# Kernel optimization log

Hardware: AMD Instinct MI355X
Metric: run time of the kernel (lower is better)

Reference implementation:

```python
import jax, jax.numpy as jnp
import numpy as np

DEPTH, DIM, HEADS, MLP, P, G, NCLS = 12, 768, 12, 3072, 16, 14, 1000
N = G * G + 1  # 197 tokens (cls + patches)
HD = DIM // HEADS
EPS = 1e-6


def _ln(x, g, b):
    m = jnp.mean(x, axis=-1, keepdims=True)
    v = jnp.var(x, axis=-1, keepdims=True)
    return (x - m) * jax.lax.rsqrt(v + EPS) * g + b


def setup_inputs() -> dict:
    key = jax.random.key(0)
    ks = jax.random.split(key, 16)
    d = {}
    d["x"] = jax.random.normal(ks[0], (32, 3, 224, 224), jnp.float32)
    d["cp_mask"] = jax.random.uniform(ks[1], (1, 1, N, N), jnp.float32)
    # patch embed conv (kernel [DIM, 3, P, P]) flattened to a matmul over (c, kh, kw)
    d["patch_w"] = jax.random.normal(ks[2], (3 * P * P, DIM), jnp.float32) * 0.02
    d["patch_b"] = jnp.zeros((DIM,), jnp.float32)
    d["cls_token"] = jax.random.normal(ks[3], (1, 1, DIM), jnp.float32) * 1e-6
    d["pos_embed"] = jax.random.normal(ks[4], (1, N, DIM), jnp.float32) * 0.02
    d["ln1_g"] = jnp.ones((DEPTH, DIM), jnp.float32)
    d["ln1_b"] = jnp.zeros((DEPTH, DIM), jnp.float32)
    d["qkv_w"] = jax.random.normal(ks[5], (DEPTH, DIM, 3 * DIM), jnp.float32) * 0.02
    d["qkv_b"] = jnp.zeros((DEPTH, 3 * DIM), jnp.float32)
    d["proj_w"] = jax.random.normal(ks[6], (DEPTH, DIM, DIM), jnp.float32) * 0.02
    d["proj_b"] = jnp.zeros((DEPTH, DIM), jnp.float32)
    d["ln2_g"] = jnp.ones((DEPTH, DIM), jnp.float32)
    d["ln2_b"] = jnp.zeros((DEPTH, DIM), jnp.float32)
    d["fc1_w"] = jax.random.normal(ks[7], (DEPTH, DIM, MLP), jnp.float32) * 0.02
    d["fc1_b"] = jnp.zeros((DEPTH, MLP), jnp.float32)
    d["fc2_w"] = jax.random.normal(ks[8], (DEPTH, MLP, DIM), jnp.float32) * 0.02
    d["fc2_b"] = jnp.zeros((DEPTH, DIM), jnp.float32)
    d["normf_g"] = jnp.ones((DIM,), jnp.float32)
    d["normf_b"] = jnp.zeros((DIM,), jnp.float32)
    d["head_w"] = jax.random.normal(ks[9], (DIM, NCLS), jnp.float32) * 0.02
    d["head_b"] = jnp.zeros((NCLS,), jnp.float32)
    return d


def vit_forward(x, cp_mask, patch_w, patch_b, cls_token, pos_embed,
                ln1_g, ln1_b, qkv_w, qkv_b, proj_w, proj_b,
                ln2_g, ln2_b, fc1_w, fc1_b, fc2_w, fc2_b,
                normf_g, normf_b, head_w, head_b):
    B = x.shape[0]
    scale = HD ** (-0.5)
    # PatchEmbed: stride-P conv == extract non-overlapping patches then matmul
    # [B,3,224,224] -> [B,3,G,P,G,P] -> [B,G,G,3,P,P] -> [B,196,3*P*P]
    patches = x.reshape(B, 3, G, P, G, P).transpose(0, 2, 4, 1, 3, 5).reshape(B, G * G, 3 * P * P)
    t = patches @ patch_w + patch_b  # [B,196,DIM]
    t = jnp.concatenate([jnp.broadcast_to(cls_token, (B, 1, DIM)), t], axis=1)
    t = t + pos_embed  # [B,197,DIM]

    for i in range(DEPTH):
        h = _ln(t, ln1_g[i], ln1_b[i])
        qkv = (h @ qkv_w[i] + qkv_b[i]).reshape(B, N, 3, HEADS, HD)
        q = qkv[:, :, 0].transpose(0, 2, 1, 3)  # [B,H,N,hd]
        k = qkv[:, :, 1].transpose(0, 2, 1, 3)
        v = qkv[:, :, 2].transpose(0, 2, 1, 3)
        attn = jnp.einsum('bhqd,bhkd->bhqk', q, k) * scale * cp_mask
        attn = jax.nn.softmax(attn, axis=-1)
        o = jnp.einsum('bhqk,bhkd->bhqd', attn, v).transpose(0, 2, 1, 3).reshape(B, N, DIM)
        t = t + (o @ proj_w[i] + proj_b[i])
        h = _ln(t, ln2_g[i], ln2_b[i])
        h = jax.nn.gelu(h @ fc1_w[i] + fc1_b[i], approximate=False)
        t = t + (h @ fc2_w[i] + fc2_b[i])

    t = _ln(t, normf_g, normf_b)
    pooled = t[:, 0]  # global_pool == 'token'
    return pooled @ head_w + head_b  # [B, NCLS]


def reference(x, cp_mask, patch_w, patch_b, cls_token, pos_embed,
              ln1_g, ln1_b, qkv_w, qkv_b, proj_w, proj_b,
              ln2_g, ln2_b, fc1_w, fc1_b, fc2_w, fc2_b,
              normf_g, normf_b, head_w, head_b):
    return vit_forward(x, cp_mask, patch_w, patch_b, cls_token, pos_embed,
                       ln1_g, ln1_b, qkv_w, qkv_b, proj_w, proj_b,
                       ln2_g, ln2_b, fc1_w, fc1_b, fc2_w, fc2_b,
                       normf_g, normf_b, head_w, head_b)
```

## Files before the change

kernel.cpp:

```cpp
#include <hip/hip_runtime.h>
#include <math.h>

#define BATCH 32
#define DEPTH 12
#define DIM 768
#define HEADS 12
#define MLP_DIM 3072
#define PATCH 16
#define GRIDSZ 14
#define NCLS 1000
#define N_TOK 197
#define HD 64
#define NPATCH 196

typedef __attribute__((ext_vector_type(8))) short short8;
typedef __attribute__((ext_vector_type(4))) float floatx4;
typedef unsigned short ushort;

__device__ inline float us2f(ushort u) {
    union { unsigned int i; float f; } c; c.i = ((unsigned int)u) << 16; return c.f;
}
__device__ inline ushort f2bf(float f) {
    unsigned int x = __float_as_uint(f);
    unsigned int r = (x + 0x7fffu + ((x >> 16) & 1u)) >> 16;
    return (ushort)r;
}

#define GAS __attribute__((address_space(1)))
#define LAS __attribute__((address_space(3)))
__device__ inline void async_copy16(const void* g, void* l) {
    __builtin_amdgcn_global_load_lds((const GAS void*)g, (LAS void*)l, 16, 0, 0);
}

__global__ __launch_bounds__(256) void im2col_kernel(const float* __restrict__ x,
                                                     ushort* __restrict__ patches) {
    int idx = blockIdx.x * 256 + threadIdx.x;
    const int total = BATCH * NPATCH * DIM;
    if (idx >= total) return;
    int e = idx % DIM;
    int n = (idx / DIM) % NPATCH;
    int b = idx / (DIM * NPATCH);
    int c = e / (PATCH * PATCH);
    int r = e % (PATCH * PATCH);
    int py = r / PATCH, px = r % PATCH;
    int gy = n / GRIDSZ, gx = n % GRIDSZ;
    size_t xi = (((size_t)(b * 3 + c) * 224 + gy * PATCH + py)) * 224 + gx * PATCH + px;
    patches[idx] = f2bf(x[xi]);
}

__global__ __launch_bounds__(256) void assemble_kernel(const float* __restrict__ patchout,
                                                       const float* __restrict__ cls,
                                                       const float* __restrict__ pos,
                                                       float* __restrict__ t) {
    int idx = blockIdx.x * 256 + threadIdx.x;
    const int total = BATCH * N_TOK * DIM;
    if (idx >= total) return;
    int d = idx % DIM;
    int n = (idx / DIM) % N_TOK;
    int b = idx / (DIM * N_TOK);
    float v = (n == 0) ? cls[d] : patchout[((size_t)b * NPATCH + (n - 1)) * DIM + d];
    t[idx] = v + pos[n * DIM + d];
}

__global__ __launch_bounds__(256) void lnw_kernel(const float* __restrict__ x,
                                                  const float* __restrict__ g,
                                                  const float* __restrict__ bta,
                                                  ushort* __restrict__ out,
                                                  int rows, int in_stride, int out_stride) {
    int w = threadIdx.x >> 6, l = threadIdx.x & 63;
    int row = blockIdx.x * 4 + w;
    if (row >= rows) return;
    const float* xr = x + (size_t)row * in_stride;
    float4 v[3];
    float s = 0.0f, s2 = 0.0f;
#pragma unroll
    for (int c = 0; c < 3; c++) {
        v[c] = *(const float4*)(xr + c * 256 + l * 4);
        s  += v[c].x + v[c].y + v[c].z + v[c].w;
        s2 += v[c].x * v[c].x + v[c].y * v[c].y + v[c].z * v[c].z + v[c].w * v[c].w;
    }
#pragma unroll
    for (int off = 32; off; off >>= 1) { s += __shfl_xor(s, off); s2 += __shfl_xor(s2, off); }
    float mean = s * (1.0f / DIM);
    float inv = rsqrtf(s2 * (1.0f / DIM) - mean * mean + 1e-6f);
    ushort* orow = out + (size_t)row * out_stride;
#pragma unroll
    for (int c = 0; c < 3; c++) {
        float4 gg = *(const float4*)(g + c * 256 + l * 4);
        float4 bb = *(const float4*)(bta + c * 256 + l * 4);
        ushort4 o4;
        o4.x = f2bf((v[c].x - mean) * inv * gg.x + bb.x);
        o4.y = f2bf((v[c].y - mean) * inv * gg.y + bb.y);
        o4.z = f2bf((v[c].z - mean) * inv * gg.z + bb.z);
        o4.w = f2bf((v[c].w - mean) * inv * gg.w + bb.w);
        *(ushort4*)(orow + c * 256 + l * 4) = o4;
    }
}

__global__ __launch_bounds__(256) void transpose_bf16_kernel(const float* __restrict__ in,
                                                             ushort* __restrict__ out,
                                                             int K, int N) {
    __shared__ float tile[32][33];
    int n0 = blockIdx.x * 32, k0 = blockIdx.y * 32;
    int tx = threadIdx.x;
    int ty = threadIdx.y;
    for (int r = ty; r < 32; r += 8) {
        int k = k0 + r, n = n0 + tx;
        tile[r][tx] = (k < K && n < N) ? in[(size_t)k * N + n] : 0.0f;
    }
    __syncthreads();
    for (int r = ty; r < 32; r += 8) {
        int n = n0 + r, k = k0 + tx;
        if (n < N && k < K) out[(size_t)n * K + k] = f2bf(tile[tx][r]);
    }
}

__global__ __launch_bounds__(256) void transpose4_kernel(
    const float* __restrict__ w0, const float* __restrict__ w1,
    const float* __restrict__ w2, const float* __restrict__ w3,
    ushort* __restrict__ o0, ushort* __restrict__ o1,
    ushort* __restrict__ o2, ushort* __restrict__ o3) {
    __shared__ float tile[32][33];
    int bid = blockIdx.x;
    const float* in; ushort* out; int K, N, nx, tl;
    if (bid < 1728)      { in = w0; out = o0; K = 768;  N = 2304; nx = 72; tl = bid; }
    else if (bid < 2304) { in = w1; out = o1; K = 768;  N = 768;  nx = 24; tl = bid - 1728; }
    else if (bid < 4608) { in = w2; out = o2; K = 768;  N = 3072; nx = 96; tl = bid - 2304; }
    else                 { in = w3; out = o3; K = 3072; N = 768;  nx = 24; tl = bid - 4608; }
    int n0 = (tl % nx) * 32, k0 = (tl / nx) * 32;
    int tx = threadIdx.x, ty = threadIdx.y;
    for (int r = ty; r < 32; r += 8)
        tile[r][tx] = in[(size_t)(k0 + r) * N + n0 + tx];
    __syncthreads();
    for (int r = ty; r < 32; r += 8)
        out[(size_t)(n0 + r) * K + k0 + tx] = f2bf(tile[tx][r]);
}

template <int BM, int GELU, int RES, int WF32, int WBF16>
__global__ __launch_bounds__(256) void gemm_bf16_mfma(
    const ushort* __restrict__ A, const ushort* __restrict__ Wt,
    const float* __restrict__ bias, const float* __restrict__ res,
    float* __restrict__ Cf, ushort* __restrict__ Cb,
    int M, int N, int K) {
    constexpr int WN = (BM == 128) ? 2 : 4;
    constexpr int FN = (BM == 128) ? 4 : 2;
    constexpr int AROWS = BM / 4;
    __shared__ short Asm[BM * 64];
    __shared__ short Bsm[128 * 64];
    const int tid = threadIdx.x;
    const int w = tid >> 6, lane = tid & 63;
    const int wm = w / WN, wn = w % WN;

    int gX = gridDim.x, gY = gridDim.y;
    int pid = blockIdx.y * gX + blockIdx.x;
    int width = 8 * gX;
    int group = pid / width;
    int first = group * 8;
    int gsz = min(gY - first, 8);
    int by = first + (pid % gsz);
    int bx = (pid % width) / gsz;
    const int m0 = by * BM, n0 = bx * 128;

    floatx4 acc[4][FN] = {};

    const int ro = lane >> 3;
    const int sl = lane & 7;
    const int gch = sl ^ ro;
    const ushort* aptr[BM / 32];
    short* alds[BM / 32];
#pragma unroll
    for (int i = 0; i < BM / 32; i++) {
        int r = w * AROWS + i * 8 + ro;
        int gr = min(m0 + r, M - 1);
        aptr[i] = A + (size_t)gr * K + gch * 8;
        alds[i] = Asm + (w * AROWS + i * 8) * 64;
    }
    const ushort* bptr[4];
    short* blds[4];
#pragma unroll
    for (int i = 0; i < 4; i++) {
        int r = w * 32 + i * 8 + ro;
        int gr = min(n0 + r, N - 1);
        bptr[i] = Wt + (size_t)gr * K + gch * 8;
        blds[i] = Bsm + (w * 32 + i * 8) * 64;
    }

    const int fr = lane & 15, quad = lane >> 4;

    for (int k0 = 0; k0 < K; k0 += 64) {
#pragma unroll
        for (int i = 0; i < BM / 32; i++) async_copy16(aptr[i] + k0, alds[i]);
#pragma unroll
        for (int i = 0; i < 4; i++) async_copy16(bptr[i] + k0, blds[i]);
        __syncthreads();
#pragma unroll
        for (int ks = 0; ks < 2; ks++) {
            int soff = (((ks * 4 + quad) ^ (fr & 7)) * 8);
            short8 af[4], bf[FN];
#pragma unroll
            for (int mt = 0; mt < 4; mt++)
                af[mt] = *(const short8*)&Asm[(wm * 64 + mt * 16 + fr) * 64 + soff];
#pragma unroll
            for (int nt = 0; nt < FN; nt++)
                bf[nt] = *(const short8*)&Bsm[(wn * (16 * FN) + nt * 16 + fr) * 64 + soff];
#pragma unroll
            for (int mt = 0; mt < 4; mt++)
#pragma unroll
                for (int nt = 0; nt < FN; nt++)
                    acc[mt][nt] = __builtin_amdgcn_mfma_f32_16x16x32_bf16(af[mt], bf[nt], acc[mt][nt], 0, 0, 0);
        }
        __syncthreads();
    }

#pragma unroll
    for (int nt = 0; nt < FN; nt++) {
        int col = n0 + wn * (16 * FN) + nt * 16 + fr;
        if (col >= N) continue;
        float bv = bias[col];
#pragma unroll
        for (int mt = 0; mt < 4; mt++) {
            int rbase = m0 + wm * 64 + mt * 16 + quad * 4;
#pragma unroll
            for (int r = 0; r < 4; r++) {
                int row = rbase + r;
                if (row >= M) continue;
                float v = acc[mt][nt][r] + bv;
                if (GELU) v = 0.5f * v * (1.0f + erff(v * 0.70710678118654752f));
                if (RES) v += res[(size_t)row * N + col];
                if (WF32) Cf[(size_t)row * N + col] = v;
                if (WBF16) Cb[(size_t)row * N + col] = f2bf(v);
            }
        }
    }
}

__global__ __launch_bounds__(256, 2) void attn_kernel(const ushort* __restrict__ qkvb,
                                                      const float* __restrict__ mask,
                                                      ushort* __restrict__ o) {
    const int h = blockIdx.x, b = blockIdx.y;
    const int tid = threadIdx.x;
    __shared__ ushort Vfrag[7 * 4 * 64 * 8];
    __shared__ ushort Pfrag[4 * 7 * 64 * 8];

    {
        uint4 z = {0, 0, 0, 0};
        uint4* v4 = (uint4*)Vfrag;
        uint4* p4 = (uint4*)Pfrag;
        for (int i = tid; i < 1792; i += 256) { v4[i] = z; p4[i] = z; }
    }
    __syncthreads();

    for (int pass = 0; pass < 25; pass++) {
        int j = pass * 8 + (tid >> 5);
        if (j <= 196) {
            int d0 = (tid & 31) * 2;
            unsigned int val = *(const unsigned int*)(qkvb + ((size_t)(b * N_TOK + j) * 3 + 2) * DIM + h * HD + d0);
            int kt = j >> 5, dt = d0 >> 4;
            int lane = ((j & 31) >> 3) * 16 + (d0 & 15);
            int jj = j & 7;
            int base = (kt * 4 + dt) * 512 + lane * 8 + jj;
            Vfrag[base] = (ushort)(val & 0xffffu);
            Vfrag[base + 8] = (ushort)(val >> 16);
        }
    }
    __syncthreads();

    const int w = tid >> 6, l = tid & 63;
    const int q = l >> 4, fr = l & 15;
    ushort* Pw = Pfrag + w * 3584;
    const float scale = 0.125f;

    for (int qt = w; qt < 13; qt += 4) {
        int qrow = min(qt * 16 + fr, 196);
        const ushort* qptr = qkvb + ((size_t)(b * N_TOK + qrow) * 3 + 0) * DIM + h * HD + q * 8;
        short8 aq0 = *(const short8*)qptr;
        short8 aq1 = *(const short8*)(qptr + 32);

        floatx4 sacc[13];
#pragma unroll
        for (int nt = 0; nt < 13; nt++) {
            int krow = min(nt * 16 + fr, 196);
            const ushort* kptr = qkvb + ((size_t)(b * N_TOK + krow) * 3 + 1) * DIM + h * HD + q * 8;
            short8 kb0 = *(const short8*)kptr;
            short8 kb1 = *(const short8*)(kptr + 32);
            floatx4 acc = {};
            acc = __builtin_amdgcn_mfma_f32_16x16x32_bf16(aq0, kb0, acc, 0, 0, 0);
            acc = __builtin_amdgcn_mfma_f32_16x16x32_bf16(aq1, kb1, acc, 0, 0, 0);
            sacc[nt] = acc;
        }

        float mx[4] = {-1e30f, -1e30f, -1e30f, -1e30f};
#pragma unroll
        for (int nt = 0; nt < 13; nt++) {
            int jcol = nt * 16 + fr;
#pragma unroll
            for (int r = 0; r < 4; r++) {
                int irow = min(qt * 16 + q * 4 + r, 196);
                float s;
                if (jcol <= 196) s = sacc[nt][r] * scale * mask[irow * N_TOK + jcol];
                else s = -1e30f;
                sacc[nt][r] = s;
                mx[r] = fmaxf(mx[r], s);
            }
        }
#pragma unroll
        for (int r = 0; r < 4; r++) {
            mx[r] = fmaxf(mx[r], __shfl_xor(mx[r], 1));
            mx[r] = fmaxf(mx[r], __shfl_xor(mx[r], 2));
            mx[r] = fmaxf(mx[r], __shfl_xor(mx[r], 4));
            mx[r] = fmaxf(mx[r], __shfl_xor(mx[r], 8));
        }

        float sum[4] = {0, 0, 0, 0};
#pragma unroll
        for (int nt = 0; nt < 13; nt++) {
            int kt = nt >> 1;
            int lpbase = ((nt & 1) * 2 + ((l & 8) >> 3)) * 16;
#pragma unroll
            for (int r = 0; r < 4; r++) {
                float e = __expf(sacc[nt][r] - mx[r]);
                sum[r] += e;
                int lp = (q * 4 + r) + lpbase;
                Pw[kt * 512 + lp * 8 + (l & 7)] = f2bf(e);
            }
        }
#pragma unroll
        for (int r = 0; r < 4; r++) {
            sum[r] += __shfl_xor(sum[r], 1);
            sum[r] += __shfl_xor(sum[r], 2);
            sum[r] += __shfl_xor(sum[r], 4);
            sum[r] += __shfl_xor(sum[r], 8);
        }

        floatx4 oacc[4] = {};
#pragma unroll
        for (int kt = 0; kt < 7; kt++) {
            short8 pa = *(const short8*)&Pw[kt * 512 + l * 8];
#pragma unroll
            for (int dt = 0; dt < 4; dt++) {
                short8 vb = *(const short8*)&Vfrag[(kt * 4 + dt) * 512 + l * 8];
                oacc[dt] = __builtin_amdgcn_mfma_f32_16x16x32_bf16(pa, vb, oacc[dt], 0, 0, 0);
            }
        }

        float inv[4];
#pragma unroll
        for (int r = 0; r < 4; r++) inv[r] = 1.0f / sum[r];
#pragma unroll
        for (int dt = 0; dt < 4; dt++) {
#pragma unroll
            for (int r = 0; r < 4; r++) {
                int irow = qt * 16 + q * 4 + r;
                if (irow <= 196)
                    o[((size_t)(b * N_TOK + irow)) * DIM + h * HD + dt * 16 + fr] = f2bf(oacc[dt][r] * inv[r]);
            }
        }
    }
}

extern "C" void kernel_launch(void* const* d_in, const int* in_sizes, int n_in,
                              void* d_out, int out_size, void* d_ws, size_t ws_size,
                              hipStream_t stream) {
    const float* x       = (const float*)d_in[0];
    const float* cp_mask = (const float*)d_in[1];
    const float* patch_w = (const float*)d_in[2];
    const float* patch_b = (const float*)d_in[3];
    const float* cls_tok = (const float*)d_in[4];
    const float* pos_emb = (const float*)d_in[5];
    const float* ln1_g   = (const float*)d_in[6];
    const float* ln1_b   = (const float*)d_in[7];
    const float* qkv_w   = (const float*)d_in[8];
    const float* qkv_b   = (const float*)d_in[9];
    const float* proj_w  = (const float*)d_in[10];
    const float* proj_b  = (const float*)d_in[11];
    const float* ln2_g   = (const float*)d_in[12];
    const float* ln2_b   = (const float*)d_in[13];
    const float* fc1_w   = (const float*)d_in[14];
    const float* fc1_b   = (const float*)d_in[15];
    const float* fc2_w   = (const float*)d_in[16];
    const float* fc2_b   = (const float*)d_in[17];
    const float* normf_g = (const float*)d_in[18];
    const float* normf_b = (const float*)d_in[19];
    const float* head_w  = (const float*)d_in[20];
    const float* head_b  = (const float*)d_in[21];
    float* out = (float*)d_out;

    const int M = BATCH * N_TOK;
    char* p = (char*)d_ws;
    auto alloc = [&](size_t bytes) { char* r = p; p += (bytes + 255) & ~(size_t)255; return r; };
    float*  t         = (float*)alloc((size_t)M * DIM * 4);
    float*  patchout  = (float*)alloc((size_t)BATCH * NPATCH * DIM * 4);
    ushort* h_bf      = (ushort*)alloc((size_t)M * DIM * 2);
    ushort* qkv_bf    = (ushort*)alloc((size_t)M * 3 * DIM * 2);
    ushort* o_bf      = (ushort*)alloc((size_t)M * DIM * 2);
    ushort* hidden_bf = (ushort*)alloc((size_t)M * MLP_DIM * 2);
    ushort* pooled_bf = (ushort*)alloc((size_t)BATCH * DIM * 2);
    ushort* wq_t      = (ushort*)alloc((size_t)3 * DIM * DIM * 2);
    ushort* wp_t      = (ushort*)alloc((size_t)DIM * DIM * 2);
    ushort* w1_t      = (ushort*)alloc((size_t)MLP_DIM * DIM * 2);
    ushort* w2_t      = (ushort*)alloc((size_t)DIM * MLP_DIM * 2);
    ushort* wpt       = (ushort*)alloc((size_t)DIM * DIM * 2);
    ushort* wht       = (ushort*)alloc((size_t)NCLS * DIM * 2);

    const dim3 tb(32, 8);

    transpose_bf16_kernel<<<dim3(24, 24), tb, 0, stream>>>(patch_w, wpt, DIM, DIM);
    transpose_bf16_kernel<<<dim3(32, 24), tb, 0, stream>>>(head_w, wht, DIM, NCLS);
    {
        int total = BATCH * NPATCH * DIM;
        im2col_kernel<<<(total + 255) / 256, 256, 0, stream>>>(x, h_bf);
        gemm_bf16_mfma<64, 0, 0, 1, 0><<<dim3(6, 98), 256, 0, stream>>>(
            h_bf, wpt, patch_b, nullptr, patchout, nullptr, BATCH * NPATCH, DIM, DIM);
        int total2 = M * DIM;
        assemble_kernel<<<(total2 + 255) / 256, 256, 0, stream>>>(patchout, cls_tok, pos_emb, t);
    }

    for (int l = 0; l < DEPTH; l++) {
        transpose4_kernel<<<6912, tb, 0, stream>>>(
            qkv_w + (size_t)l * DIM * 3 * DIM, proj_w + (size_t)l * DIM * DIM,
            fc1_w + (size_t)l * DIM * MLP_DIM, fc2_w + (size_t)l * MLP_DIM * DIM,
            wq_t, wp_t, w1_t, w2_t);

        lnw_kernel<<<M / 4, 256, 0, stream>>>(t, ln1_g + l * DIM, ln1_b + l * DIM, h_bf, M, DIM, DIM);

        gemm_bf16_mfma<128, 0, 0, 0, 1><<<dim3(18, 50), 256, 0, stream>>>(
            h_bf, wq_t, qkv_b + (size_t)l * 3 * DIM, nullptr, nullptr, qkv_bf, M, 3 * DIM, DIM);

        attn_kernel<<<dim3(HEADS, BATCH), 256, 0, stream>>>(qkv_bf, cp_mask, o_bf);

        gemm_bf16_mfma<64, 0, 1, 1, 0><<<dim3(6, 99), 256, 0, stream>>>(
            o_bf, wp_t, proj_b + (size_t)l * DIM, t, t, nullptr, M, DIM, DIM);

        lnw_kernel<<<M / 4, 256, 0, stream>>>(t, ln2_g + l * DIM, ln2_b + l * DIM, h_bf, M, DIM, DIM);

        gemm_bf16_mfma<128, 1, 0, 0, 1><<<dim3(24, 50), 256, 0, stream>>>(
            h_bf, w1_t, fc1_b + (size_t)l * MLP_DIM, nullptr, nullptr, hidden_bf, M, MLP_DIM, DIM);

        gemm_bf16_mfma<64, 0, 1, 1, 0><<<dim3(6, 99), 256, 0, stream>>>(
            hidden_bf, w2_t, fc2_b + (size_t)l * DIM, t, t, nullptr, M, DIM, MLP_DIM);
    }

    lnw_kernel<<<8, 256, 0, stream>>>(t, normf_g, normf_b, pooled_bf, BATCH, N_TOK * DIM, DIM);
    gemm_bf16_mfma<64, 0, 0, 1, 0><<<dim3(8, 1), 256, 0, stream>>>(
        pooled_bf, wht, head_b, nullptr, out, nullptr, BATCH, NCLS, DIM);
}
```

Baseline: 3.361 ms.

## Double-buffer GEMM LDS tiles to overlap async loads with MFMA compute

The bf16 MFMA GEMM now keeps two LDS buffers for the A and B tiles. It issues async global-to-LDS copies for the next K step before computing the current one, and uses explicit vmcnt waits plus raw s_barrier in place of __syncthreads. The goal is to hide global load latency behind the matrix-core work. The cost is doubled LDS use, which can lower occupancy, and the hand-written waitcnt values must match the exact number of copies issued per step.

Result: slower. 3.452 ms (+2.7%).

```diff
diff --git a/kernel.cpp b/kernel.cpp
--- a/kernel.cpp
+++ b/kernel.cpp
@@ -145,8 +145,10 @@
     constexpr int WN = (BM == 128) ? 2 : 4;
     constexpr int FN = (BM == 128) ? 4 : 2;
     constexpr int AROWS = BM / 4;
-    __shared__ short Asm[BM * 64];
-    __shared__ short Bsm[128 * 64];
+    constexpr int ABUF = BM * 64;
+    constexpr int BBUF = 128 * 64;
+    __shared__ short Asm[2 * ABUF];
+    __shared__ short Bsm[2 * BBUF];
     const int tid = threadIdx.x;
     const int w = tid >> 6, lane = tid & 63;
     const int wm = w / WN, wn = w % WN;
@@ -187,29 +189,48 @@
 
     const int fr = lane & 15, quad = lane >> 4;
 
-    for (int k0 = 0; k0 < K; k0 += 64) {
-#pragma unroll
-        for (int i = 0; i < BM / 32; i++) async_copy16(aptr[i] + k0, alds[i]);
-#pragma unroll
-        for (int i = 0; i < 4; i++) async_copy16(bptr[i] + k0, blds[i]);
-        __syncthreads();
+    const int nsteps = K >> 6;
+#pragma unroll
+    for (int i = 0; i < BM / 32; i++) async_copy16(aptr[i], alds[i]);
+#pragma unroll
+    for (int i = 0; i < 4; i++) async_copy16(bptr[i], blds[i]);
+
+    int cur = 0;
+    for (int t = 0; t < nsteps; ++t) {
+        if (t + 1 < nsteps) {
+            const int nxt = cur ^ 1;
+            const int kk = (t + 1) << 6;
+#pragma unroll
+            for (int i = 0; i < BM / 32; i++) async_copy16(aptr[i] + kk, alds[i] + nxt * ABUF);
+#pragma unroll
+            for (int i = 0; i < 4; i++) async_copy16(bptr[i] + kk, blds[i] + nxt * BBUF);
+            if constexpr (BM == 128) asm volatile("s_waitcnt vmcnt(8)" ::: "memory");
+            else                     asm volatile("s_waitcnt vmcnt(6)" ::: "memory");
+        } else {
+            asm volatile("s_waitcnt vmcnt(0)" ::: "memory");
+        }
+        asm volatile("s_barrier" ::: "memory");
+
+        const short* As = Asm + cur * ABUF;
+        const short* Bs = Bsm + cur * BBUF;
 #pragma unroll
         for (int ks = 0; ks < 2; ks++) {
             int soff = (((ks * 4 + quad) ^ (fr & 7)) * 8);
             short8 af[4], bf[FN];
 #pragma unroll
             for (int mt = 0; mt < 4; mt++)
-                af[mt] = *(const short8*)&Asm[(wm * 64 + mt * 16 + fr) * 64 + soff];
+                af[mt] = *(const short8*)&As[(wm * 64 + mt * 16 + fr) * 64 + soff];
 #pragma unroll
             for (int nt = 0; nt < FN; nt++)
-                bf[nt] = *(const short8*)&Bsm[(wn * (16 * FN) + nt * 16 + fr) * 64 + soff];
+                bf[nt] = *(const short8*)&Bs[(wn * (16 * FN) + nt * 16 + fr) * 64 + soff];
 #pragma unroll
             for (int mt = 0; mt < 4; mt++)
 #pragma unroll
                 for (int nt = 0; nt < FN; nt++)
                     acc[mt][nt] = __builtin_amdgcn_mfma_f32_16x16x32_bf16(af[mt], bf[nt], acc[mt][nt], 0, 0, 0);
         }
-        __syncthreads();
+        asm volatile("s_barrier" ::: "memory");
+        cur ^= 1;
     }
 
 #pragma unroll
```
